# Kernel tuning notes

Measured on AMD Instinct MI355X. Metric: run time of the kernel, lower is better.

Reference implementation:

```python
import jax
import jax.numpy as jnp
from jax import lax
import numpy as np

MAX_Q = 127.0  # 2**(8-1) - 1, signed int8 symmetric


def setup_inputs() -> dict:
    key = jax.random.key(0)
    kx, kw, kb = jax.random.split(key, 3)
    x = jax.random.normal(kx, (32, 8, 384, 384), dtype=jnp.float32)
    weight = jax.random.normal(kw, (8, 8, 3, 3), dtype=jnp.float32) * 0.1
    bias = jax.random.normal(kb, (8,), dtype=jnp.float32) * 0.01
    return {"x": x, "weight": weight, "bias": bias}


def _quantize(v, scale):
    # per-tensor symmetric int8 quantization: round, clip to [-127, 127]
    return jnp.clip(jnp.round(v * scale), -MAX_Q, MAX_Q)


def reference(x, weight, bias):
    # calibrated per-tensor amax == abs-max of the tensor
    sx = MAX_Q / jnp.max(jnp.abs(x))
    sw = MAX_Q / jnp.max(jnp.abs(weight))
    qx = _quantize(x, sx)       # int values in [-127,127], kept in fp32 (exact)
    qw = _quantize(weight, sw)
    # exact int conv (systolic kernel, use_exact=True): products <= 127^2,
    # K = 8*3*3 = 72 terms -> max |accum| ~ 1.16e6 << 2^24, exact in fp32.
    out_i32 = lax.conv_general_dilated(
        qx, qw,
        window_strides=(1, 1),
        padding=[(1, 1), (1, 1)],
        lhs_dilation=(1, 1),
        rhs_dilation=(1, 1),
        dimension_numbers=("NCHW", "OIHW", "NCHW"),
    )
    out = out_i32 / (sx * sw)   # dequantize: scale = (127/amax_x)*(127/amax_w)
    return out + bias[None, :, None, None]
```

## Files before the change

### kernel.cpp

```cpp
#include <hip/hip_runtime.h>

#define PLANE (384 * 384)
#define TH 16
#define TW 64
#define TROWS 18
#define TCOLS 66

#if __has_builtin(__builtin_amdgcn_sdot4)
__device__ __forceinline__ int sdot4(int a, int b, int c) {
    return __builtin_amdgcn_sdot4(a, b, c, false);
}
#else
__device__ __forceinline__ int sdot4(int a, int b, int c) {
    #pragma unroll
    for (int i = 0; i < 4; ++i)
        c += ((a << (24 - 8 * i)) >> 24) * ((b << (24 - 8 * i)) >> 24);
    return c;
}
#endif

__global__ __launch_bounds__(256) void amax_kernel(
    const float* __restrict__ x, const float* __restrict__ w,
    unsigned int* __restrict__ ws)
{
    __shared__ float red[4];
    const long n4 = 9437184;
    long tid = (long)blockIdx.x * blockDim.x + threadIdx.x;
    long stride = (long)gridDim.x * blockDim.x;
    const float4* x4 = (const float4*)x;

    float m = 0.f;
    for (long i = tid; i < n4; i += stride) {
        float4 v = x4[i];
        m = fmaxf(m, fmaxf(fmaxf(fabsf(v.x), fabsf(v.y)),
                           fmaxf(fabsf(v.z), fabsf(v.w))));
    }
    #pragma unroll
    for (int off = 32; off > 0; off >>= 1)
        m = fmaxf(m, __shfl_down(m, off, 64));
    if ((threadIdx.x & 63) == 0) red[threadIdx.x >> 6] = m;
    __syncthreads();
    if (threadIdx.x == 0) {
        float bm = fmaxf(fmaxf(red[0], red[1]), fmaxf(red[2], red[3]));
        atomicMax(&ws[0], __float_as_uint(bm));
    }

    if (blockIdx.x == 0) {
        float mw = 0.f;
        for (int j = threadIdx.x; j < 576; j += 256)
            mw = fmaxf(mw, fabsf(w[j]));
        #pragma unroll
        for (int off = 32; off > 0; off >>= 1)
            mw = fmaxf(mw, __shfl_down(mw, off, 64));
        if ((threadIdx.x & 63) == 0)
            atomicMax(&ws[1], __float_as_uint(mw));
    }
}

__global__ __launch_bounds__(256) void conv_kernel(
    const float* __restrict__ x, const float* __restrict__ w,
    const float* __restrict__ bias, const unsigned int* __restrict__ ws,
    float* __restrict__ out)
{
    __shared__ __align__(16) unsigned sIn[TROWS * TCOLS * 2];
    __shared__ __align__(16) unsigned sWq[9 * 8 * 2];
    __shared__ float sB[8];

    const float amax_x = __uint_as_float(ws[0]);
    const float amax_w = __uint_as_float(ws[1]);
    const float s_x = 127.0f / amax_x;
    const float s_w = 127.0f / amax_w;
    const float inv = 1.0f / (s_x * s_w);

    const int bid = blockIdx.x;
    const int bx = bid % 6;
    const int by = (bid / 6) % 24;
    const int n  = bid / (6 * 24);
    const int h0 = by * TH;
    const int w0 = bx * TW;
    const int tid = threadIdx.x;

    if (tid < 144) {
        int h = tid & 1, k = (tid >> 1) & 7, p = tid >> 4;
        unsigned pk = 0;
        #pragma unroll
        for (int j = 0; j < 4; ++j) {
            int c = 4 * h + j;
            float qv = fminf(fmaxf(rintf(w[k * 72 + c * 9 + p] * s_w), -127.f), 127.f);
            int qi = (int)qv;
            pk |= ((unsigned)(qi & 0xff)) << (8 * j);
        }
        sWq[p * 16 + k * 2 + h] = pk;
    }
    if (tid < 8) sB[tid] = bias[tid];

    const float* xn = x + (long)n * 8 * PLANE;
    for (int q = tid; q < TROWS * TCOLS; q += 256) {
        int yy = q / TCOLS;
        int xx = q - yy * TCOLS;
        int gy = h0 - 1 + yy;
        int gx = w0 - 1 + xx;
        bool ok = ((unsigned)gy < 384u) && ((unsigned)gx < 384u);
        long base = (long)gy * 384 + gx;
        unsigned lo = 0, hi = 0;
        #pragma unroll
        for (int c = 0; c < 8; ++c) {
            float v = 0.f;
            if (ok) v = xn[(long)c * PLANE + base];
            float qv = fminf(fmaxf(rintf(v * s_x), -127.f), 127.f);
            int qi = (int)qv;
            if (c < 4) lo |= ((unsigned)(qi & 0xff)) << (8 * c);
            else       hi |= ((unsigned)(qi & 0xff)) << (8 * (c - 4));
        }
        *(uint2*)&sIn[2 * q] = make_uint2(lo, hi);
    }
    __syncthreads();

    const int ty = tid >> 4;
    const int tx = tid & 15;

    int acc[4][8];
    #pragma unroll
    for (int i = 0; i < 4; ++i)
        #pragma unroll
        for (int k = 0; k < 8; ++k) acc[i][k] = 0;

    #pragma unroll
    for (int r = 0; r < 3; ++r) {
        const uint4* ip = (const uint4*)&sIn[((ty + r) * TCOLS + 4 * tx) * 2];
        uint4 i0 = ip[0], i1 = ip[1], i2 = ip[2];
        unsigned d[12] = {i0.x, i0.y, i0.z, i0.w,
                          i1.x, i1.y, i1.z, i1.w,
                          i2.x, i2.y, i2.z, i2.w};
        #pragma unroll
        for (int s = 0; s < 3; ++s) {
            const uint4* wp = (const uint4*)&sWq[(r * 3 + s) * 16];
            uint4 wa = wp[0], wb = wp[1], wc = wp[2], wd = wp[3];
            unsigned wk[16] = {wa.x, wa.y, wa.z, wa.w, wb.x, wb.y, wb.z, wb.w,
                               wc.x, wc.y, wc.z, wc.w, wd.x, wd.y, wd.z, wd.w};
            #pragma unroll
            for (int k = 0; k < 8; ++k)
                #pragma unroll
                for (int i = 0; i < 4; ++i)
                    acc[i][k] = sdot4((int)d[2 * (i + s) + 1], (int)wk[2 * k + 1],
                                sdot4((int)d[2 * (i + s)],     (int)wk[2 * k],
                                      acc[i][k]));
        }
    }

    float* on = out + (long)n * 8 * PLANE + (long)(h0 + ty) * 384 + (w0 + 4 * tx);
    #pragma unroll
    for (int k = 0; k < 8; ++k) {
        float4 o;
        o.x = fmaf((float)acc[0][k], inv, sB[k]);
        o.y = fmaf((float)acc[1][k], inv, sB[k]);
        o.z = fmaf((float)acc[2][k], inv, sB[k]);
        o.w = fmaf((float)acc[3][k], inv, sB[k]);
        *(float4*)(on + (long)k * PLANE) = o;
    }
}

extern "C" void kernel_launch(void* const* d_in, const int* in_sizes, int n_in,
                              void* d_out, int out_size, void* d_ws, size_t ws_size,
                              hipStream_t stream) {
    const float* x   = (const float*)d_in[0];
    const float* w   = (const float*)d_in[1];
    const float* b   = (const float*)d_in[2];
    float* out       = (float*)d_out;
    unsigned int* ws = (unsigned int*)d_ws;

    hipMemsetAsync(ws, 0, 2 * sizeof(unsigned int), stream);
    amax_kernel<<<2048, 256, 0, stream>>>(x, w, ws);
    conv_kernel<<<32 * 24 * 6, 256, 0, stream>>>(x, w, b, ws, out);
}
```

Measured before the change: 323.0 us.

## Vectorize conv halo-tile loads, unroll amax loop, use nontemporal output stores

The conv tile loader now has each thread fetch float4 spans of a row across all 8 channels, replacing scalar per-pixel loads. The left and right halo columns are handled separately by 36 threads using scalar loads. The amax kernel loop is fully unrolled with a fixed trip count tied to the grid size, and output stores become nontemporal to avoid polluting cache. Together these aim to cut global load instruction count and issue overhead, at the cost of hardcoding the grid and tile geometry.

```diff
diff --git a/kernel.cpp b/kernel.cpp
--- a/kernel.cpp
+++ b/kernel.cpp
@@ -6,6 +6,8 @@
 #define TROWS 18
 #define TCOLS 66
 
+typedef float f4_t __attribute__((ext_vector_type(4)));
+
 #if __has_builtin(__builtin_amdgcn_sdot4)
 __device__ __forceinline__ int sdot4(int a, int b, int c) {
     return __builtin_amdgcn_sdot4(a, b, c, false);
@@ -24,14 +26,13 @@
     unsigned int* __restrict__ ws)
 {
     __shared__ float red[4];
-    const long n4 = 9437184;
-    long tid = (long)blockIdx.x * blockDim.x + threadIdx.x;
-    long stride = (long)gridDim.x * blockDim.x;
     const float4* x4 = (const float4*)x;
+    const int tid = blockIdx.x * 256 + threadIdx.x;
 
     float m = 0.f;
-    for (long i = tid; i < n4; i += stride) {
-        float4 v = x4[i];
+    #pragma unroll
+    for (int i = 0; i < 18; ++i) {
+        float4 v = x4[tid + i * 524288];
         m = fmaxf(m, fmaxf(fmaxf(fabsf(v.x), fabsf(v.y)),
                            fmaxf(fabsf(v.z), fabsf(v.w))));
     }
@@ -95,24 +96,53 @@
     if (tid < 8) sB[tid] = bias[tid];
 
     const float* xn = x + (long)n * 8 * PLANE;
-    for (int q = tid; q < TROWS * TCOLS; q += 256) {
-        int yy = q / TCOLS;
-        int xx = q - yy * TCOLS;
+
+    for (int task = tid; task < 288; task += 256) {
+        int yy = task >> 4;
+        int g  = task & 15;
+        int gy = h0 - 1 + yy;
+        bool rowok = ((unsigned)gy < 384u);
+        const float* rp = xn + (long)gy * 384 + (w0 + 4 * g);
+        unsigned lo[4] = {0, 0, 0, 0}, hi[4] = {0, 0, 0, 0};
+        if (rowok) {
+            #pragma unroll
+            for (int c = 0; c < 8; ++c) {
+                f4_t v = *(const f4_t*)(rp + (long)c * PLANE);
+                #pragma unroll
+                for (int j = 0; j < 4; ++j) {
+                    float qv = fminf(fmaxf(rintf(v[j] * s_x), -127.f), 127.f);
+                    int qi = (int)qv;
+                    unsigned b = ((unsigned)(qi & 0xff)) << (8 * (c & 3));
+                    if (c < 4) lo[j] |= b; else hi[j] |= b;
+                }
+            }
+        }
+        int q0 = yy * TCOLS + 1 + 4 * g;
+        #pragma unroll
+        for (int j = 0; j < 4; ++j)
+            *(uint2*)&sIn[2 * (q0 + j)] = make_uint2(lo[j], hi[j]);
+    }
+
+    if (tid >= 220) {
+        int t = tid - 220;
+        int yy = t >> 1;
+        int xx = (t & 1) ? 65 : 0;
         int gy = h0 - 1 + yy;
         int gx = w0 - 1 + xx;
         bool ok = ((unsigned)gy < 384u) && ((unsigned)gx < 384u);
         long base = (long)gy * 384 + gx;
         unsigned lo = 0, hi = 0;
-        #pragma unroll
-        for (int c = 0; c < 8; ++c) {
-            float v = 0.f;
-            if (ok) v = xn[(long)c * PLANE + base];
-            float qv = fminf(fmaxf(rintf(v * s_x), -127.f), 127.f);
-            int qi = (int)qv;
-            if (c < 4) lo |= ((unsigned)(qi & 0xff)) << (8 * c);
-            else       hi |= ((unsigned)(qi & 0xff)) << (8 * (c - 4));
-        }
-        *(uint2*)&sIn[2 * q] = make_uint2(lo, hi);
+        if (ok) {
+            #pragma unroll
+            for (int c = 0; c < 8; ++c) {
+                float v = xn[(long)c * PLANE + base];
+                float qv = fminf(fmaxf(rintf(v * s_x), -127.f), 127.f);
+                int qi = (int)qv;
+                if (c < 4) lo |= ((unsigned)(qi & 0xff)) << (8 * c);
+                else       hi |= ((unsigned)(qi & 0xff)) << (8 * (c - 4));
+            }
+        }
+        *(uint2*)&sIn[2 * (yy * TCOLS + xx)] = make_uint2(lo, hi);
     }
     __syncthreads();
 
@@ -151,12 +181,12 @@
     float* on = out + (long)n * 8 * PLANE + (long)(h0 + ty) * 384 + (w0 + 4 * tx);
     #pragma unroll
     for (int k = 0; k < 8; ++k) {
-        float4 o;
+        f4_t o;
         o.x = fmaf((float)acc[0][k], inv, sB[k]);
         o.y = fmaf((float)acc[1][k], inv, sB[k]);
         o.z = fmaf((float)acc[2][k], inv, sB[k]);
         o.w = fmaf((float)acc[3][k], inv, sB[k]);
-        *(float4*)(on + (long)k * PLANE) = o;
+        __builtin_nontemporal_store(o, (f4_t*)(on + (long)k * PLANE));
     }
 }
 
```

Measured after the change: 308.9 us. 4.4% less time.
